# Optimization experiments

Measured on AMD Instinct MI355X. Metric: run time of the kernel, lower is better.

Reference implementation:

```python
import jax, jax.numpy as jnp
import numpy as np

N = 10000      # nodes
E = 320000     # edges (before self-loops)
IN_DIM = 128
HID = 64
OUT = 32
HEADS = 8
NEG_SLOPE = 0.2  # PyG GATConv default leaky_relu slope


def gat_conv(x, W, a_src, a_dst, b, src, dst, num_nodes, heads, d):
    """One PyG-style GATConv layer (eval mode, concat=True).
    x: [N, F_in], W: [F_in, heads*d], a_src/a_dst: [heads, d], b: [heads*d]
    src/dst: [E'] int edge endpoints (self-loops already included).
    """
    h = (x @ W).reshape(num_nodes, heads, d)              # [N, H, D]
    alpha_s = jnp.sum(h * a_src, axis=-1)                 # [N, H]
    alpha_d = jnp.sum(h * a_dst, axis=-1)                 # [N, H]
    logits = jax.nn.leaky_relu(alpha_s[src] + alpha_d[dst], NEG_SLOPE)  # [E', H]
    # segment softmax over incoming edges of each destination node
    m = jax.lax.stop_gradient(
        jax.ops.segment_max(logits, dst, num_segments=num_nodes))      # [N, H]
    e = jnp.exp(logits - m[dst])                          # [E', H]
    denom = jax.ops.segment_sum(e, dst, num_segments=num_nodes)        # [N, H]
    alpha = e / denom[dst]                                # [E', H]
    out = jax.ops.segment_sum(alpha[:, :, None] * h[src], dst,
                              num_segments=num_nodes)     # [N, H, D]
    return out.reshape(num_nodes, heads * d) + b


def setup_inputs() -> dict:
    key = jax.random.key(0)
    ks = jax.random.split(key, 10)
    x = jax.random.normal(ks[0], (N, IN_DIM), jnp.float32)
    edge_index = jax.random.randint(ks[1], (2, E), 0, N, dtype=jnp.int64)
    s1 = 1.0 / np.sqrt(IN_DIM)
    W1 = jax.random.normal(ks[2], (IN_DIM, HEADS * HID), jnp.float32) * s1
    a1_src = jax.random.normal(ks[3], (HEADS, HID), jnp.float32) * 0.1
    a1_dst = jax.random.normal(ks[4], (HEADS, HID), jnp.float32) * 0.1
    b1 = jnp.zeros((HEADS * HID,), jnp.float32)
    s2 = 1.0 / np.sqrt(HEADS * HID)
    W2 = jax.random.normal(ks[5], (HEADS * HID, OUT), jnp.float32) * s2
    a2_src = jax.random.normal(ks[6], (1, OUT), jnp.float32) * 0.1
    a2_dst = jax.random.normal(ks[7], (1, OUT), jnp.float32) * 0.1
    b2 = jnp.zeros((OUT,), jnp.float32)
    return {"x": x, "edge_index": edge_index,
            "W1": W1, "a1_src": a1_src, "a1_dst": a1_dst, "b1": b1,
            "W2": W2, "a2_src": a2_src, "a2_dst": a2_dst, "b2": b2}


def reference(x, edge_index, W1, a1_src, a1_dst, b1, W2, a2_src, a2_dst, b2):
    # add self-loops (PyG GATConv default add_self_loops=True)
    loops = jnp.arange(N, dtype=edge_index.dtype)
    src = jnp.concatenate([edge_index[0], loops])
    dst = jnp.concatenate([edge_index[1], loops])
    # dropout layers are identity in eval mode
    h = gat_conv(x, W1, a1_src, a1_dst, b1, src, dst, N, HEADS, HID)
    h = jax.nn.elu(h)
    out = gat_conv(h, W2, a2_src, a2_dst, b2, src, dst, N, 1, OUT)
    return out
```

## Files before the change

kernel.cpp:

```cpp
#include <hip/hip_runtime.h>
#include <math.h>

#define N_NODES 10000
#define E_EDGES 320000
#define EA      (E_EDGES + N_NODES)
#define IN_DIM  128
#define HID     512
#define HEADS   8
#define OUT_DIM 32
#define NEG     0.2f
#define CAP     160
#define KSPLIT  384
#define N_PAD   10048
#define NRB     628
#define RB_SH   6144

#define ZB   40
#define PXB  5024
#define PWB  256
#define SCB  645

typedef __attribute__((ext_vector_type(8))) short bf16x8;
typedef __attribute__((ext_vector_type(4))) float f32x4;

__device__ __forceinline__ float leaky(float x){ return x > 0.f ? x : NEG * x; }

__device__ __forceinline__ unsigned short bf16rn(float x){
    unsigned int b = __float_as_uint(x);
    b += 0x7fffu + ((b >> 16) & 1u);
    return (unsigned short)(b >> 16);
}

__device__ __forceinline__ size_t frag_off(int rb, int kk, int l15){
    int ks  = kk >> 5;
    int grp = (kk >> 3) & 3;
    int el  = kk & 7;
    return ((size_t)rb * RB_SH) + ((ks * 4 + grp) * 16 + l15) * 8 + el;
}

__global__ void k_pre(const float* __restrict__ x, const float* __restrict__ W1,
                      int* __restrict__ cnt,
                      unsigned short* __restrict__ Ax, unsigned short* __restrict__ Bt){
    int b = blockIdx.x, t = threadIdx.x;
    if (b < ZB){
        int i = b * 256 + t;
        if (i < N_NODES) cnt[i] = 0;
    } else if (b < ZB + PXB){
        int idx = (b - ZB) * 256 + t;
        int n = idx >> 7, k = idx & 127;
        float v = (n < N_NODES) ? x[(size_t)n * IN_DIM + k] : 0.f;
        unsigned short hi = bf16rn(v);
        float vhi = __uint_as_float((unsigned)hi << 16);
        unsigned short lo = bf16rn(v - vhi);
        int rb = n >> 4, l15 = n & 15;
        Ax[frag_off(rb, k, l15)]       = hi;
        Ax[frag_off(rb, 128 + k, l15)] = lo;
        Ax[frag_off(rb, 256 + k, l15)] = hi;
    } else {
        int idx = (b - ZB - PXB) * 256 + t;
        int nn = idx >> 7, k = idx & 127;
        float v = W1[(size_t)k * HID + nn];
        unsigned short hi = bf16rn(v);
        float vhi = __uint_as_float((unsigned)hi << 16);
        unsigned short lo = bf16rn(v - vhi);
        int nb = nn >> 4, l15 = nn & 15;
        Bt[frag_off(nb, k, l15)]       = hi;
        Bt[frag_off(nb, 128 + k, l15)] = hi;
        Bt[frag_off(nb, 256 + k, l15)] = lo;
    }
}

__launch_bounds__(512)
__global__ void k_sg(const int* __restrict__ eidx, int* __restrict__ cnt,
                     int* __restrict__ esrc,
                     const unsigned short* __restrict__ Ax,
                     const unsigned short* __restrict__ Bt,
                     const float* __restrict__ a1s, const float* __restrict__ a1d,
                     unsigned short* __restrict__ h1,
                     float* __restrict__ as1, float* __restrict__ ad1){
    if (blockIdx.x < SCB){
        int e = blockIdx.x * 512 + threadIdx.x;
        if (e < EA){
            int d, s;
            if (e < E_EDGES){ s = eidx[e]; d = eidx[E_EDGES + e]; }
            else { s = d = e - E_EDGES; }
            int pos = atomicAdd(&cnt[d], 1);
            if (pos < CAP) esrc[d * CAP + pos] = s;
        }
        return;
    }
    int rb = blockIdx.x - SCB;
    int by = threadIdx.x >> 6;
    int lane = threadIdx.x & 63;
    int l15 = lane & 15, grp = lane >> 4;
    int m0 = rb * 16;
    int n0 = by * 64;
    const unsigned short* ap = Ax + (size_t)rb * RB_SH + (size_t)lane * 8;
    bf16x8 a[12];
#pragma unroll
    for (int ks = 0; ks < 12; ks++)
        a[ks] = *reinterpret_cast<const bf16x8*>(ap + ks * 512);
    const unsigned short* bp = Bt + (size_t)(by * 4) * RB_SH + (size_t)lane * 8;
    f32x4 acc[4] = {};
#pragma unroll
    for (int ks = 0; ks < 12; ks++){
#pragma unroll
        for (int ns = 0; ns < 4; ns++){
            bf16x8 b = *reinterpret_cast<const bf16x8*>(bp + (size_t)ns * RB_SH + ks * 512);
            acc[ns] = __builtin_amdgcn_mfma_f32_16x16x32_bf16(a[ks], b, acc[ns], 0, 0, 0);
        }
    }
    float vs[4] = {0.f, 0.f, 0.f, 0.f}, vd[4] = {0.f, 0.f, 0.f, 0.f};
#pragma unroll
    for (int ns = 0; ns < 4; ns++){
        int c = n0 + ns * 16 + l15;
        float a_s = a1s[c], a_d = a1d[c];
#pragma unroll
        for (int r = 0; r < 4; r++){
            float v = acc[ns][r];
            int rr = m0 + grp * 4 + r;
            if (rr < N_NODES) h1[(size_t)rr * HID + c] = bf16rn(v);
            vs[r] += v * a_s; vd[r] += v * a_d;
        }
    }
#pragma unroll
    for (int r = 0; r < 4; r++){
#pragma unroll
        for (int off = 8; off >= 1; off >>= 1){
            vs[r] += __shfl_xor(vs[r], off);
            vd[r] += __shfl_xor(vd[r], off);
        }
    }
    if (l15 == 0){
#pragma unroll
        for (int r = 0; r < 4; r++){
            int rr = m0 + grp * 4 + r;
            if (rr < N_NODES){ as1[rr * HEADS + by] = vs[r]; ad1[rr * HEADS + by] = vd[r]; }
        }
    }
}

__launch_bounds__(128)
__global__ void k_agg1(const unsigned short* __restrict__ h1,
                       const float* __restrict__ as1, const float* __restrict__ ad1,
                       const int* __restrict__ cnt, const int* __restrict__ esrc,
                       const float* __restrict__ b1, float* __restrict__ h1b){
    int n = blockIdx.x;
    int c = cnt[n]; if (c > CAP) c = CAP;
    int beg = n * CAP;
    int t = threadIdx.x;
    __shared__ int   s_src[CAP];
    __shared__ float s_w[HEADS][CAP + 1];
    __shared__ float s_adn[HEADS];
    __shared__ float s_red[2][HEADS];
    __shared__ float s_m[HEADS];
    if (t < HEADS) s_adn[t] = ad1[n * HEADS + t];
    __syncthreads();
    float pm[HEADS];
#pragma unroll
    for (int h = 0; h < HEADS; h++) pm[h] = -INFINITY;
    for (int i = t; i < c; i += 128){
        int s = esrc[beg + i];
        float4 alo = *reinterpret_cast<const float4*>(as1 + (size_t)s * HEADS);
        float4 ahi = *reinterpret_cast<const float4*>(as1 + (size_t)s * HEADS + 4);
        float lg[HEADS];
        lg[0] = leaky(alo.x + s_adn[0]); lg[1] = leaky(alo.y + s_adn[1]);
        lg[2] = leaky(alo.z + s_adn[2]); lg[3] = leaky(alo.w + s_adn[3]);
        lg[4] = leaky(ahi.x + s_adn[4]); lg[5] = leaky(ahi.y + s_adn[5]);
        lg[6] = leaky(ahi.z + s_adn[6]); lg[7] = leaky(ahi.w + s_adn[7]);
        s_src[i] = s;
#pragma unroll
        for (int h = 0; h < HEADS; h++){ s_w[h][i] = lg[h]; pm[h] = fmaxf(pm[h], lg[h]); }
    }
#pragma unroll
    for (int h = 0; h < HEADS; h++)
#pragma unroll
        for (int off = 32; off >= 1; off >>= 1)
            pm[h] = fmaxf(pm[h], __shfl_down(pm[h], off));
    int wv = t >> 6;
    if ((t & 63) == 0)
#pragma unroll
        for (int h = 0; h < HEADS; h++) s_red[wv][h] = pm[h];
    __syncthreads();
    if (t < HEADS) s_m[t] = fmaxf(s_red[0][t], s_red[1][t]);
    __syncthreads();
    for (int i = t; i < c; i += 128){
#pragma unroll
        for (int h = 0; h < HEADS; h++) s_w[h][i] = __expf(s_w[h][i] - s_m[h]);
    }
    __syncthreads();
    int d0 = 4 * t;
    int h = t >> 4;
    float a0a = 0.f, a1a = 0.f, a2a = 0.f, a3a = 0.f, dena = 0.f;
    float a0b = 0.f, a1b = 0.f, a2b = 0.f, a3b = 0.f, denb = 0.f;
    int i = 0;
    for (; i + 1 < c; i += 2){
        float wa = s_w[h][i];     int sa = s_src[i];
        float wb = s_w[h][i + 1]; int sb = s_src[i + 1];
        uint2 hva = *reinterpret_cast<const uint2*>(h1 + (size_t)sa * HID + d0);
        uint2 hvb = *reinterpret_cast<const uint2*>(h1 + (size_t)sb * HID + d0);
        a0a += wa * __uint_as_float(hva.x << 16);
        a1a += wa * __uint_as_float(hva.x & 0xffff0000u);
        a2a += wa * __uint_as_float(hva.y << 16);
        a3a += wa * __uint_as_float(hva.y & 0xffff0000u);
        dena += wa;
        a0b += wb * __uint_as_float(hvb.x << 16);
        a1b += wb * __uint_as_float(hvb.x & 0xffff0000u);
        a2b += wb * __uint_as_float(hvb.y << 16);
        a3b += wb * __uint_as_float(hvb.y & 0xffff0000u);
        denb += wb;
    }
    if (i < c){
        float w = s_w[h][i]; int s = s_src[i];
        uint2 hv = *reinterpret_cast<const uint2*>(h1 + (size_t)s * HID + d0);
        a0a += w * __uint_as_float(hv.x << 16);
        a1a += w * __uint_as_float(hv.x & 0xffff0000u);
        a2a += w * __uint_as_float(hv.y << 16);
        a3a += w * __uint_as_float(hv.y & 0xffff0000u);
        dena += w;
    }
    float acc0 = a0a + a0b, acc1 = a1a + a1b, acc2 = a2a + a2b, acc3 = a3a + a3b;
    float den = dena + denb;
    float4 bv = *reinterpret_cast<const float4*>(b1 + d0);
    float rd = 1.f / den;
    float o0 = acc0 * rd + bv.x;
    float o1 = acc1 * rd + bv.y;
    float o2 = acc2 * rd + bv.z;
    float o3 = acc3 * rd + bv.w;
    float4 o;
    o.x = o0 > 0.f ? o0 : expm1f(o0);
    o.y = o1 > 0.f ? o1 : expm1f(o1);
    o.z = o2 > 0.f ? o2 : expm1f(o2);
    o.w = o3 > 0.f ? o3 : expm1f(o3);
    *reinterpret_cast<float4*>(h1b + (size_t)n * HID + d0) = o;
}

__launch_bounds__(128)
__global__ void k_gemm2(const float* __restrict__ h1b, const float* __restrict__ W2,
                        const float* __restrict__ a2s, const float* __restrict__ a2d,
                        float* __restrict__ h2, float* __restrict__ as2,
                        float* __restrict__ ad2){
    __shared__ float hs[16 * 516];
    int t = threadIdx.x;
    int n0 = blockIdx.x * 16;
    const float4* src = reinterpret_cast<const float4*>(h1b + (size_t)n0 * HID);
    for (int i = t; i < 2048; i += 128){
        int r = i >> 7, c4 = i & 127;
        *reinterpret_cast<float4*>(&hs[r * 516 + c4 * 4]) = src[i];
    }
    __syncthreads();
    int nl = t >> 3, cg = t & 7, c0 = cg * 4;
    float a0 = 0.f, a1 = 0.f, a2 = 0.f, a3 = 0.f;
#pragma unroll 2
    for (int k4 = 0; k4 < 128; k4++){
        float4 hv = *reinterpret_cast<const float4*>(&hs[nl * 516 + k4 * 4]);
        float4 w0 = *reinterpret_cast<const float4*>(W2 + (k4 * 4 + 0) * OUT_DIM + c0);
        float4 w1 = *reinterpret_cast<const float4*>(W2 + (k4 * 4 + 1) * OUT_DIM + c0);
        float4 w2 = *reinterpret_cast<const float4*>(W2 + (k4 * 4 + 2) * OUT_DIM + c0);
        float4 w3 = *reinterpret_cast<const float4*>(W2 + (k4 * 4 + 3) * OUT_DIM + c0);
        a0 += hv.x * w0.x + hv.y * w1.x + hv.z * w2.x + hv.w * w3.x;
        a1 += hv.x * w0.y + hv.y * w1.y + hv.z * w2.y + hv.w * w3.y;
        a2 += hv.x * w0.z + hv.y * w1.z + hv.z * w2.z + hv.w * w3.z;
        a3 += hv.x * w0.w + hv.y * w1.w + hv.z * w2.w + hv.w * w3.w;
    }
    float4 o; o.x = a0; o.y = a1; o.z = a2; o.w = a3;
    *reinterpret_cast<float4*>(h2 + (size_t)(n0 + nl) * OUT_DIM + c0) = o;
    float4 s4 = *reinterpret_cast<const float4*>(a2s + c0);
    float4 d4 = *reinterpret_cast<const float4*>(a2d + c0);
    float vs = a0 * s4.x + a1 * s4.y + a2 * s4.z + a3 * s4.w;
    float vd = a0 * d4.x + a1 * d4.y + a2 * d4.z + a3 * d4.w;
#pragma unroll
    for (int off = 4; off >= 1; off >>= 1){
        vs += __shfl_xor(vs, off);
        vd += __shfl_xor(vd, off);
    }
    if (cg == 0){ as2[n0 + nl] = vs; ad2[n0 + nl] = vd; }
}

__launch_bounds__(256)
__global__ void k_agg2(const float* __restrict__ h2, const float* __restrict__ as2,
                       const float* __restrict__ ad2, const int* __restrict__ cnt,
                       const int* __restrict__ esrc,
                       const float* __restrict__ b2, float* __restrict__ out){
    int wv = threadIdx.x >> 6;
    int lane = threadIdx.x & 63;
    int n = blockIdx.x * 4 + wv;
    __shared__ float s_w[4][CAP];
    __shared__ int   s_src[4][CAP];
    int c = cnt[n]; if (c > CAP) c = CAP;
    int beg = n * CAP;
    float adn = ad2[n];
    float pm = -INFINITY;
    for (int i = lane; i < c; i += 64){
        int s = esrc[beg + i];
        float lg = leaky(as2[s] + adn);
        s_src[wv][i] = s; s_w[wv][i] = lg;
        pm = fmaxf(pm, lg);
    }
#pragma unroll
    for (int off = 32; off >= 1; off >>= 1)
        pm = fmaxf(pm, __shfl_xor(pm, off));
    __syncthreads();
    for (int i = lane; i < c; i += 64) s_w[wv][i] = __expf(s_w[wv][i] - pm);
    __syncthreads();
    int d = lane & 31, half = lane >> 5;
    float acc = 0.f, den = 0.f;
    for (int i = half; i < c; i += 2){
        float w = s_w[wv][i]; int s = s_src[wv][i];
        acc += w * h2[(size_t)s * OUT_DIM + d];
        den += w;
    }
    acc += __shfl_xor(acc, 32);
    den += __shfl_xor(den, 32);
    if (lane < OUT_DIM) out[(size_t)n * OUT_DIM + d] = acc / den + b2[d];
}

extern "C" void kernel_launch(void* const* d_in, const int* in_sizes, int n_in,
                              void* d_out, int out_size, void* d_ws, size_t ws_size,
                              hipStream_t stream){
    const float* x   = (const float*)d_in[0];
    const int*  eidx = (const int*)  d_in[1];
    const float* W1  = (const float*)d_in[2];
    const float* a1s = (const float*)d_in[3];
    const float* a1d = (const float*)d_in[4];
    const float* b1  = (const float*)d_in[5];
    const float* W2  = (const float*)d_in[6];
    const float* a2s = (const float*)d_in[7];
    const float* a2d = (const float*)d_in[8];
    const float* b2  = (const float*)d_in[9];
    float* out = (float*)d_out;

    char* ws = (char*)d_ws;
    size_t off = 0;
    auto alloc = [&](size_t bytes) -> void* {
        void* p = ws + off;
        off += (bytes + 255) & ~(size_t)255;
        return p;
    };
    unsigned short* h1 = (unsigned short*)alloc((size_t)N_NODES * HID * 2);
    float* h1b  = (float*)alloc((size_t)N_NODES * HID * 4);
    float* as1  = (float*)alloc((size_t)N_NODES * HEADS * 4);
    float* ad1  = (float*)alloc((size_t)N_NODES * HEADS * 4);
    float* h2   = (float*)alloc((size_t)N_NODES * OUT_DIM * 4);
    float* vs2  = (float*)alloc((size_t)N_NODES * 4);
    float* vd2  = (float*)alloc((size_t)N_NODES * 4);
    int* cnt    = (int*)alloc((size_t)N_NODES * 4);
    int* esrc   = (int*)alloc((size_t)N_NODES * CAP * 4);
    unsigned short* Bt = (unsigned short*)alloc((size_t)32 * RB_SH * 2);
    unsigned short* Ax = (unsigned short*)h1b;

    k_pre <<<ZB + PXB + PWB, 256, 0, stream>>>(x, W1, cnt, Ax, Bt);
    k_sg  <<<SCB + NRB, 512, 0, stream>>>(eidx, cnt, esrc, Ax, Bt, a1s, a1d,
                                          h1, as1, ad1);
    k_agg1<<<N_NODES, 128, 0, stream>>>(h1, as1, ad1, cnt, esrc, b1, h1b);
    k_gemm2<<<N_NODES / 16, 128, 0, stream>>>(h1b, W2, a2s, a2d, h2, vs2, vd2);
    k_agg2<<<N_NODES / 4, 256, 0, stream>>>(h2, vs2, vd2, cnt, esrc, b2, out);
}
```

Baseline: 132.8 us.

## Fuse layer-2 GEMM into aggregation and store split-bf16 hi/lo operands compactly

Folds the second-layer projection (h1 row times W2) into the first aggregation kernel, using a pre-transposed W2 copy, so the fp32 h1b intermediate is never written and read back and one launch is dropped. The preprocessing kernel now stages x and W1 tiles through shared memory and writes packed 16-byte hi/lo fragments. It stores hi and lo once each instead of three duplicated slices. The GEMM issues three MFMAs per step, reusing registers for the split terms. The fused per-node matvec adds work to each aggregation block, and this may cost occupancy.

New measurement: 155.9 us. 17.3% more time.

```diff
diff --git a/kernel.cpp b/kernel.cpp
--- a/kernel.cpp
+++ b/kernel.cpp
@@ -10,14 +10,13 @@
 #define OUT_DIM 32
 #define NEG     0.2f
 #define CAP     160
-#define KSPLIT  384
 #define N_PAD   10048
 #define NRB     628
-#define RB_SH   6144
-
-#define ZB   40
-#define PXB  5024
-#define PWB  256
+#define RB_SH   4096
+
+#define PWB  32
+#define PTB  64
+#define ZBK  40
 #define SCB  645
 
 typedef __attribute__((ext_vector_type(8))) short bf16x8;
@@ -31,42 +30,74 @@
     return (unsigned short)(b >> 16);
 }
 
-__device__ __forceinline__ size_t frag_off(int rb, int kk, int l15){
-    int ks  = kk >> 5;
-    int grp = (kk >> 3) & 3;
-    int el  = kk & 7;
-    return ((size_t)rb * RB_SH) + ((ks * 4 + grp) * 16 + l15) * 8 + el;
-}
-
 __global__ void k_pre(const float* __restrict__ x, const float* __restrict__ W1,
-                      int* __restrict__ cnt,
-                      unsigned short* __restrict__ Ax, unsigned short* __restrict__ Bt){
+                      const float* __restrict__ W2, int* __restrict__ cnt,
+                      unsigned short* __restrict__ Ax, unsigned short* __restrict__ Bt,
+                      float* __restrict__ W2T){
     int b = blockIdx.x, t = threadIdx.x;
-    if (b < ZB){
-        int i = b * 256 + t;
+    if (b < NRB){
+        __shared__ float xs[16 * 132];
+        int rb = b;
+#pragma unroll
+        for (int j = 0; j < 2; j++){
+            int idx = t + j * 256;
+            int r = idx >> 5, c4 = idx & 31;
+            int row = rb * 16 + r;
+            float4 v = make_float4(0.f, 0.f, 0.f, 0.f);
+            if (row < N_NODES)
+                v = *reinterpret_cast<const float4*>(x + (size_t)row * IN_DIM + c4 * 4);
+            *reinterpret_cast<float4*>(&xs[r * 132 + c4 * 4]) = v;
+        }
+        __syncthreads();
+        int l15 = t & 15, kk8 = t >> 4;
+        unsigned short hi[8], lo[8];
+#pragma unroll
+        for (int el = 0; el < 8; el++){
+            float f = xs[l15 * 132 + kk8 * 8 + el];
+            hi[el] = bf16rn(f);
+            lo[el] = bf16rn(f - __uint_as_float((unsigned)hi[el] << 16));
+        }
+        uint4 H, L;
+        H.x = hi[0] | ((unsigned)hi[1] << 16); H.y = hi[2] | ((unsigned)hi[3] << 16);
+        H.z = hi[4] | ((unsigned)hi[5] << 16); H.w = hi[6] | ((unsigned)hi[7] << 16);
+        L.x = lo[0] | ((unsigned)lo[1] << 16); L.y = lo[2] | ((unsigned)lo[3] << 16);
+        L.z = lo[4] | ((unsigned)lo[5] << 16); L.w = lo[6] | ((unsigned)lo[7] << 16);
+        unsigned short* base = Ax + (size_t)rb * RB_SH;
+        *reinterpret_cast<uint4*>(base + (kk8 * 16 + l15) * 8) = H;
+        *reinterpret_cast<uint4*>(base + 2048 + (kk8 * 16 + l15) * 8) = L;
+    } else if (b < NRB + PWB){
+        __shared__ float ws[128 * 17];
+        int nb = b - NRB;
+        int j = t & 15, kr = t >> 4;
+#pragma unroll
+        for (int it = 0; it < 8; it++){
+            int k = it * 16 + kr;
+            ws[k * 17 + j] = W1[(size_t)k * HID + nb * 16 + j];
+        }
+        __syncthreads();
+        int l15 = t & 15, kk8 = t >> 4;
+        unsigned short hi[8], lo[8];
+#pragma unroll
+        for (int el = 0; el < 8; el++){
+            float f = ws[(kk8 * 8 + el) * 17 + l15];
+            hi[el] = bf16rn(f);
+            lo[el] = bf16rn(f - __uint_as_float((unsigned)hi[el] << 16));
+        }
+        uint4 H, L;
+        H.x = hi[0] | ((unsigned)hi[1] << 16); H.y = hi[2] | ((unsigned)hi[3] << 16);
+        H.z = hi[4] | ((unsigned)hi[5] << 16); H.w = hi[6] | ((unsigned)hi[7] << 16);
+        L.x = lo[0] | ((unsigned)lo[1] << 16); L.y = lo[2] | ((unsigned)lo[3] << 16);
+        L.z = lo[4] | ((unsigned)lo[5] << 16); L.w = lo[6] | ((unsigned)lo[7] << 16);
+        unsigned short* base = Bt + (size_t)nb * RB_SH;
+        *reinterpret_cast<uint4*>(base + (kk8 * 16 + l15) * 8) = H;
+        *reinterpret_cast<uint4*>(base + 2048 + (kk8 * 16 + l15) * 8) = L;
+    } else if (b < NRB + PWB + PTB){
+        int idx = (b - NRB - PWB) * 256 + t;
+        int k = idx & 511, c = idx >> 9;
+        W2T[(size_t)c * HID + k] = W2[(size_t)k * OUT_DIM + c];
+    } else {
+        int i = (b - NRB - PWB - PTB) * 256 + t;
         if (i < N_NODES) cnt[i] = 0;
-    } else if (b < ZB + PXB){
-        int idx = (b - ZB) * 256 + t;
-        int n = idx >> 7, k = idx & 127;
-        float v = (n < N_NODES) ? x[(size_t)n * IN_DIM + k] : 0.f;
-        unsigned short hi = bf16rn(v);
-        float vhi = __uint_as_float((unsigned)hi << 16);
-        unsigned short lo = bf16rn(v - vhi);
-        int rb = n >> 4, l15 = n & 15;
-        Ax[frag_off(rb, k, l15)]       = hi;
-        Ax[frag_off(rb, 128 + k, l15)] = lo;
-        Ax[frag_off(rb, 256 + k, l15)] = hi;
-    } else {
-        int idx = (b - ZB - PXB) * 256 + t;
-        int nn = idx >> 7, k = idx & 127;
-        float v = W1[(size_t)k * HID + nn];
-        unsigned short hi = bf16rn(v);
-        float vhi = __uint_as_float((unsigned)hi << 16);
-        unsigned short lo = bf16rn(v - vhi);
-        int nb = nn >> 4, l15 = nn & 15;
-        Bt[frag_off(nb, k, l15)]       = hi;
-        Bt[frag_off(nb, 128 + k, l15)] = hi;
-        Bt[frag_off(nb, 256 + k, l15)] = lo;
     }
 }
 
@@ -96,18 +127,24 @@
     int m0 = rb * 16;
     int n0 = by * 64;
     const unsigned short* ap = Ax + (size_t)rb * RB_SH + (size_t)lane * 8;
-    bf16x8 a[12];
-#pragma unroll
-    for (int ks = 0; ks < 12; ks++)
-        a[ks] = *reinterpret_cast<const bf16x8*>(ap + ks * 512);
+    bf16x8 a_hi[4], a_lo[4];
+#pragma unroll
+    for (int ks = 0; ks < 4; ks++){
+        a_hi[ks] = *reinterpret_cast<const bf16x8*>(ap + ks * 512);
+        a_lo[ks] = *reinterpret_cast<const bf16x8*>(ap + 2048 + ks * 512);
+    }
     const unsigned short* bp = Bt + (size_t)(by * 4) * RB_SH + (size_t)lane * 8;
     f32x4 acc[4] = {};
 #pragma unroll
-    for (int ks = 0; ks < 12; ks++){
+    for (int ks = 0; ks < 4; ks++){
 #pragma unroll
         for (int ns = 0; ns < 4; ns++){
-            bf16x8 b = *reinterpret_cast<const bf16x8*>(bp + (size_t)ns * RB_SH + ks * 512);
-            acc[ns] = __builtin_amdgcn_mfma_f32_16x16x32_bf16(a[ks], b, acc[ns], 0, 0, 0);
+            const unsigned short* bb = bp + (size_t)ns * RB_SH + ks * 512;
+            bf16x8 b_hi = *reinterpret_cast<const bf16x8*>(bb);
+            bf16x8 b_lo = *reinterpret_cast<const bf16x8*>(bb + 2048);
+            acc[ns] = __builtin_amdgcn_mfma_f32_16x16x32_bf16(a_hi[ks], b_hi, acc[ns], 0, 0, 0);
+            acc[ns] = __builtin_amdgcn_mfma_f32_16x16x32_bf16(a_lo[ks], b_hi, acc[ns], 0, 0, 0);
+            acc[ns] = __builtin_amdgcn_mfma_f32_16x16x32_bf16(a_hi[ks], b_lo, acc[ns], 0, 0, 0);
         }
     }
     float vs[4] = {0.f, 0.f, 0.f, 0.f}, vd[4] = {0.f, 0.f, 0.f, 0.f};
@@ -144,7 +181,10 @@
 __global__ void k_agg1(const unsigned short* __restrict__ h1,
                        const float* __restrict__ as1, const float* __restrict__ ad1,
                        const int* __restrict__ cnt, const int* __restrict__ esrc,
-                       const float* __restrict__ b1, float* __restrict__ h1b){
+                       const float* __restrict__ b1, const float* __restrict__ W2T,
+                       const float* __restrict__ a2s, const float* __restrict__ a2d,
+                       float* __restrict__ h2, float* __restrict__ vs2,
+                       float* __restrict__ vd2){
     int n = blockIdx.x;
     int c = cnt[n]; if (c > CAP) c = CAP;
     int beg = n * CAP;
@@ -154,6 +194,8 @@
     __shared__ float s_adn[HEADS];
     __shared__ float s_red[2][HEADS];
     __shared__ float s_m[HEADS];
+    __shared__ float s_row[HID];
+    __shared__ float s_p[4][OUT_DIM];
     if (t < HEADS) s_adn[t] = ad1[n * HEADS + t];
     __syncthreads();
     float pm[HEADS];
@@ -191,90 +233,67 @@
     __syncthreads();
     int d0 = 4 * t;
     int h = t >> 4;
-    float a0a = 0.f, a1a = 0.f, a2a = 0.f, a3a = 0.f, dena = 0.f;
-    float a0b = 0.f, a1b = 0.f, a2b = 0.f, a3b = 0.f, denb = 0.f;
+    float ac[4][4] = {}, dn[4] = {};
     int i = 0;
-    for (; i + 1 < c; i += 2){
-        float wa = s_w[h][i];     int sa = s_src[i];
-        float wb = s_w[h][i + 1]; int sb = s_src[i + 1];
-        uint2 hva = *reinterpret_cast<const uint2*>(h1 + (size_t)sa * HID + d0);
-        uint2 hvb = *reinterpret_cast<const uint2*>(h1 + (size_t)sb * HID + d0);
-        a0a += wa * __uint_as_float(hva.x << 16);
-        a1a += wa * __uint_as_float(hva.x & 0xffff0000u);
-        a2a += wa * __uint_as_float(hva.y << 16);
-        a3a += wa * __uint_as_float(hva.y & 0xffff0000u);
-        dena += wa;
-        a0b += wb * __uint_as_float(hvb.x << 16);
-        a1b += wb * __uint_as_float(hvb.x & 0xffff0000u);
-        a2b += wb * __uint_as_float(hvb.y << 16);
-        a3b += wb * __uint_as_float(hvb.y & 0xffff0000u);
-        denb += wb;
-    }
-    if (i < c){
+    for (; i + 3 < c; i += 4){
+#pragma unroll
+        for (int u = 0; u < 4; u++){
+            float w = s_w[h][i + u]; int s = s_src[i + u];
+            uint2 hv = *reinterpret_cast<const uint2*>(h1 + (size_t)s * HID + d0);
+            ac[u][0] += w * __uint_as_float(hv.x << 16);
+            ac[u][1] += w * __uint_as_float(hv.x & 0xffff0000u);
+            ac[u][2] += w * __uint_as_float(hv.y << 16);
+            ac[u][3] += w * __uint_as_float(hv.y & 0xffff0000u);
+            dn[u] += w;
+        }
+    }
+    for (; i < c; i++){
         float w = s_w[h][i]; int s = s_src[i];
         uint2 hv = *reinterpret_cast<const uint2*>(h1 + (size_t)s * HID + d0);
-        a0a += w * __uint_as_float(hv.x << 16);
-        a1a += w * __uint_as_float(hv.x & 0xffff0000u);
-        a2a += w * __uint_as_float(hv.y << 16);
-        a3a += w * __uint_as_float(hv.y & 0xffff0000u);
-        dena += w;
-    }
-    float acc0 = a0a + a0b, acc1 = a1a + a1b, acc2 = a2a + a2b, acc3 = a3a + a3b;
-    float den = dena + denb;
+        ac[0][0] += w * __uint_as_float(hv.x << 16);
+        ac[0][1] += w * __uint_as_float(hv.x & 0xffff0000u);
+        ac[0][2] += w * __uint_as_float(hv.y << 16);
+        ac[0][3] += w * __uint_as_float(hv.y & 0xffff0000u);
+        dn[0] += w;
+    }
+    float den = (dn[0] + dn[1]) + (dn[2] + dn[3]);
+    float rd = 1.f / den;
     float4 bv = *reinterpret_cast<const float4*>(b1 + d0);
-    float rd = 1.f / den;
-    float o0 = acc0 * rd + bv.x;
-    float o1 = acc1 * rd + bv.y;
-    float o2 = acc2 * rd + bv.z;
-    float o3 = acc3 * rd + bv.w;
+    float o0 = ((ac[0][0] + ac[1][0]) + (ac[2][0] + ac[3][0])) * rd + bv.x;
+    float o1 = ((ac[0][1] + ac[1][1]) + (ac[2][1] + ac[3][1])) * rd + bv.y;
+    float o2 = ((ac[0][2] + ac[1][2]) + (ac[2][2] + ac[3][2])) * rd + bv.z;
+    float o3 = ((ac[0][3] + ac[1][3]) + (ac[2][3] + ac[3][3])) * rd + bv.w;
     float4 o;
     o.x = o0 > 0.f ? o0 : expm1f(o0);
     o.y = o1 > 0.f ? o1 : expm1f(o1);
     o.z = o2 > 0.f ? o2 : expm1f(o2);
     o.w = o3 > 0.f ? o3 : expm1f(o3);
-    *reinterpret_cast<float4*>(h1b + (size_t)n * HID + d0) = o;
-}
-
-__launch_bounds__(128)
-__global__ void k_gemm2(const float* __restrict__ h1b, const float* __restrict__ W2,
-                        const float* __restrict__ a2s, const float* __restrict__ a2d,
-                        float* __restrict__ h2, float* __restrict__ as2,
-                        float* __restrict__ ad2){
-    __shared__ float hs[16 * 516];
-    int t = threadIdx.x;
-    int n0 = blockIdx.x * 16;
-    const float4* src = reinterpret_cast<const float4*>(h1b + (size_t)n0 * HID);
-    for (int i = t; i < 2048; i += 128){
-        int r = i >> 7, c4 = i & 127;
-        *reinterpret_cast<float4*>(&hs[r * 516 + c4 * 4]) = src[i];
-    }
-    __syncthreads();
-    int nl = t >> 3, cg = t & 7, c0 = cg * 4;
-    float a0 = 0.f, a1 = 0.f, a2 = 0.f, a3 = 0.f;
-#pragma unroll 2
-    for (int k4 = 0; k4 < 128; k4++){
-        float4 hv = *reinterpret_cast<const float4*>(&hs[nl * 516 + k4 * 4]);
-        float4 w0 = *reinterpret_cast<const float4*>(W2 + (k4 * 4 + 0) * OUT_DIM + c0);
-        float4 w1 = *reinterpret_cast<const float4*>(W2 + (k4 * 4 + 1) * OUT_DIM + c0);
-        float4 w2 = *reinterpret_cast<const float4*>(W2 + (k4 * 4 + 2) * OUT_DIM + c0);
-        float4 w3 = *reinterpret_cast<const float4*>(W2 + (k4 * 4 + 3) * OUT_DIM + c0);
-        a0 += hv.x * w0.x + hv.y * w1.x + hv.z * w2.x + hv.w * w3.x;
-        a1 += hv.x * w0.y + hv.y * w1.y + hv.z * w2.y + hv.w * w3.y;
-        a2 += hv.x * w0.z + hv.y * w1.z + hv.z * w2.z + hv.w * w3.z;
-        a3 += hv.x * w0.w + hv.y * w1.w + hv.z * w2.w + hv.w * w3.w;
-    }
-    float4 o; o.x = a0; o.y = a1; o.z = a2; o.w = a3;
-    *reinterpret_cast<float4*>(h2 + (size_t)(n0 + nl) * OUT_DIM + c0) = o;
-    float4 s4 = *reinterpret_cast<const float4*>(a2s + c0);
-    float4 d4 = *reinterpret_cast<const float4*>(a2d + c0);
-    float vs = a0 * s4.x + a1 * s4.y + a2 * s4.z + a3 * s4.w;
-    float vd = a0 * d4.x + a1 * d4.y + a2 * d4.z + a3 * d4.w;
-#pragma unroll
-    for (int off = 4; off >= 1; off >>= 1){
-        vs += __shfl_xor(vs, off);
-        vd += __shfl_xor(vd, off);
-    }
-    if (cg == 0){ as2[n0 + nl] = vs; ad2[n0 + nl] = vd; }
+    *reinterpret_cast<float4*>(&s_row[d0]) = o;
+    __syncthreads();
+    int cc = t & 31, q = t >> 5;
+    const float4* wr = reinterpret_cast<const float4*>(W2T + (size_t)cc * HID + q * 128);
+    const float4* rr = reinterpret_cast<const float4*>(&s_row[q * 128]);
+    float p = 0.f;
+#pragma unroll 8
+    for (int kk = 0; kk < 32; kk++){
+        float4 rv = rr[kk];
+        float4 wv = wr[kk];
+        p += rv.x * wv.x + rv.y * wv.y + rv.z * wv.z + rv.w * wv.w;
+    }
+    s_p[q][cc] = p;
+    __syncthreads();
+    if (t < OUT_DIM){
+        float h2c = (s_p[0][t] + s_p[1][t]) + (s_p[2][t] + s_p[3][t]);
+        h2[(size_t)n * OUT_DIM + t] = h2c;
+        float vs = h2c * a2s[t];
+        float vd = h2c * a2d[t];
+#pragma unroll
+        for (int off = 16; off >= 1; off >>= 1){
+            vs += __shfl_xor(vs, off);
+            vd += __shfl_xor(vd, off);
+        }
+        if (t == 0){ vs2[n] = vs; vd2[n] = vd; }
+    }
 }
 
 __launch_bounds__(256)
@@ -338,7 +357,9 @@
         return p;
     };
     unsigned short* h1 = (unsigned short*)alloc((size_t)N_NODES * HID * 2);
-    float* h1b  = (float*)alloc((size_t)N_NODES * HID * 4);
+    unsigned short* Ax = (unsigned short*)alloc((size_t)NRB * RB_SH * 2);
+    unsigned short* Bt = (unsigned short*)alloc((size_t)32 * RB_SH * 2);
+    float* W2T  = (float*)alloc((size_t)OUT_DIM * HID * 4);
     float* as1  = (float*)alloc((size_t)N_NODES * HEADS * 4);
     float* ad1  = (float*)alloc((size_t)N_NODES * HEADS * 4);
     float* h2   = (float*)alloc((size_t)N_NODES * OUT_DIM * 4);
@@ -346,13 +367,11 @@
     float* vd2  = (float*)alloc((size_t)N_NODES * 4);
     int* cnt    = (int*)alloc((size_t)N_NODES * 4);
     int* esrc   = (int*)alloc((size_t)N_NODES * CAP * 4);
-    unsigned short* Bt = (unsigned short*)alloc((size_t)32 * RB_SH * 2);
-    unsigned short* Ax = (unsigned short*)h1b;
-
-    k_pre <<<ZB + PXB + PWB, 256, 0, stream>>>(x, W1, cnt, Ax, Bt);
+
+    k_pre <<<NRB + PWB + PTB + ZBK, 256, 0, stream>>>(x, W1, W2, cnt, Ax, Bt, W2T);
     k_sg  <<<SCB + NRB, 512, 0, stream>>>(eidx, cnt, esrc, Ax, Bt, a1s, a1d,
                                           h1, as1, ad1);
-    k_agg1<<<N_NODES, 128, 0, stream>>>(h1, as1, ad1, cnt, esrc, b1, h1b);
-    k_gemm2<<<N_NODES / 16, 128, 0, stream>>>(h1b, W2, a2s, a2d, h2, vs2, vd2);
+    k_agg1<<<N_NODES, 128, 0, stream>>>(h1, as1, ad1, cnt, esrc, b1, W2T,
+                                        a2s, a2d, h2, vs2, vd2);
     k_agg2<<<N_NODES / 4, 256, 0, stream>>>(h2, vs2, vd2, cnt, esrc, b2, out);
 }
```

## Store hi/lo bf16 split once and vectorize fragment packing via shared memory

Applied to the files above, without the earlier changes.

The preprocessing kernel now stages x and W1 tiles in shared memory and writes packed 16-byte MFMA fragments, replacing per-element scattered 2-byte stores. The triplicated K=384 layout (hi,lo,hi / hi,hi,lo) is replaced by a K=256 hi/lo layout. The GEMM issues the three split-bf16 MFMAs explicitly per k-step. This shrinks the fragment buffers and cuts uncoalesced writes in the prep kernel, at the cost of extra shared-memory staging and a barrier.

Result: faster. 126.8 us (-4.5%).

```diff
diff --git a/kernel.cpp b/kernel.cpp
--- a/kernel.cpp
+++ b/kernel.cpp
@@ -10,14 +10,12 @@
 #define OUT_DIM 32
 #define NEG     0.2f
 #define CAP     160
-#define KSPLIT  384
 #define N_PAD   10048
 #define NRB     628
-#define RB_SH   6144
-
-#define ZB   40
-#define PXB  5024
-#define PWB  256
+#define RB_SH   4096
+
+#define PWB  32
+#define ZBK  40
 #define SCB  645
 
 typedef __attribute__((ext_vector_type(8))) short bf16x8;
@@ -31,42 +29,69 @@
     return (unsigned short)(b >> 16);
 }
 
-__device__ __forceinline__ size_t frag_off(int rb, int kk, int l15){
-    int ks  = kk >> 5;
-    int grp = (kk >> 3) & 3;
-    int el  = kk & 7;
-    return ((size_t)rb * RB_SH) + ((ks * 4 + grp) * 16 + l15) * 8 + el;
-}
-
 __global__ void k_pre(const float* __restrict__ x, const float* __restrict__ W1,
                       int* __restrict__ cnt,
                       unsigned short* __restrict__ Ax, unsigned short* __restrict__ Bt){
     int b = blockIdx.x, t = threadIdx.x;
-    if (b < ZB){
-        int i = b * 256 + t;
+    if (b < NRB){
+        __shared__ float xs[16 * 132];
+        int rb = b;
+#pragma unroll
+        for (int j = 0; j < 2; j++){
+            int idx = t + j * 256;
+            int r = idx >> 5, c4 = idx & 31;
+            int row = rb * 16 + r;
+            float4 v = make_float4(0.f, 0.f, 0.f, 0.f);
+            if (row < N_NODES)
+                v = *reinterpret_cast<const float4*>(x + (size_t)row * IN_DIM + c4 * 4);
+            *reinterpret_cast<float4*>(&xs[r * 132 + c4 * 4]) = v;
+        }
+        __syncthreads();
+        int l15 = t & 15, kk8 = t >> 4;
+        unsigned short hi[8], lo[8];
+#pragma unroll
+        for (int el = 0; el < 8; el++){
+            float f = xs[l15 * 132 + kk8 * 8 + el];
+            hi[el] = bf16rn(f);
+            lo[el] = bf16rn(f - __uint_as_float((unsigned)hi[el] << 16));
+        }
+        uint4 H, L;
+        H.x = hi[0] | ((unsigned)hi[1] << 16); H.y = hi[2] | ((unsigned)hi[3] << 16);
+        H.z = hi[4] | ((unsigned)hi[5] << 16); H.w = hi[6] | ((unsigned)hi[7] << 16);
+        L.x = lo[0] | ((unsigned)lo[1] << 16); L.y = lo[2] | ((unsigned)lo[3] << 16);
+        L.z = lo[4] | ((unsigned)lo[5] << 16); L.w = lo[6] | ((unsigned)lo[7] << 16);
+        unsigned short* base = Ax + (size_t)rb * RB_SH;
+        *reinterpret_cast<uint4*>(base + (kk8 * 16 + l15) * 8) = H;
+        *reinterpret_cast<uint4*>(base + 2048 + (kk8 * 16 + l15) * 8) = L;
+    } else if (b < NRB + PWB){
+        __shared__ float wsh[128 * 17];
+        int nb = b - NRB;
+        int j = t & 15, kr = t >> 4;
+#pragma unroll
+        for (int it = 0; it < 8; it++){
+            int k = it * 16 + kr;
+            wsh[k * 17 + j] = W1[(size_t)k * HID + nb * 16 + j];
+        }
+        __syncthreads();
+        int l15 = t & 15, kk8 = t >> 4;
+        unsigned short hi[8], lo[8];
+#pragma unroll
+        for (int el = 0; el < 8; el++){
+            float f = wsh[(kk8 * 8 + el) * 17 + l15];
+            hi[el] = bf16rn(f);
+            lo[el] = bf16rn(f - __uint_as_float((unsigned)hi[el] << 16));
+        }
+        uint4 H, L;
+        H.x = hi[0] | ((unsigned)hi[1] << 16); H.y = hi[2] | ((unsigned)hi[3] << 16);
+        H.z = hi[4] | ((unsigned)hi[5] << 16); H.w = hi[6] | ((unsigned)hi[7] << 16);
+        L.x = lo[0] | ((unsigned)lo[1] << 16); L.y = lo[2] | ((unsigned)lo[3] << 16);
+        L.z = lo[4] | ((unsigned)lo[5] << 16); L.w = lo[6] | ((unsigned)lo[7] << 16);
+        unsigned short* base = Bt + (size_t)nb * RB_SH;
+        *reinterpret_cast<uint4*>(base + (kk8 * 16 + l15) * 8) = H;
+        *reinterpret_cast<uint4*>(base + 2048 + (kk8 * 16 + l15) * 8) = L;
+    } else {
+        int i = (b - NRB - PWB) * 256 + t;
         if (i < N_NODES) cnt[i] = 0;
-    } else if (b < ZB + PXB){
-        int idx = (b - ZB) * 256 + t;
-        int n = idx >> 7, k = idx & 127;
-        float v = (n < N_NODES) ? x[(size_t)n * IN_DIM + k] : 0.f;
-        unsigned short hi = bf16rn(v);
-        float vhi = __uint_as_float((unsigned)hi << 16);
-        unsigned short lo = bf16rn(v - vhi);
-        int rb = n >> 4, l15 = n & 15;
-        Ax[frag_off(rb, k, l15)]       = hi;
-        Ax[frag_off(rb, 128 + k, l15)] = lo;
-        Ax[frag_off(rb, 256 + k, l15)] = hi;
-    } else {
-        int idx = (b - ZB - PXB) * 256 + t;
-        int nn = idx >> 7, k = idx & 127;
-        float v = W1[(size_t)k * HID + nn];
-        unsigned short hi = bf16rn(v);
-        float vhi = __uint_as_float((unsigned)hi << 16);
-        unsigned short lo = bf16rn(v - vhi);
-        int nb = nn >> 4, l15 = nn & 15;
-        Bt[frag_off(nb, k, l15)]       = hi;
-        Bt[frag_off(nb, 128 + k, l15)] = hi;
-        Bt[frag_off(nb, 256 + k, l15)] = lo;
     }
 }
 
@@ -96,18 +121,24 @@
     int m0 = rb * 16;
     int n0 = by * 64;
     const unsigned short* ap = Ax + (size_t)rb * RB_SH + (size_t)lane * 8;
-    bf16x8 a[12];
-#pragma unroll
-    for (int ks = 0; ks < 12; ks++)
-        a[ks] = *reinterpret_cast<const bf16x8*>(ap + ks * 512);
+    bf16x8 a_hi[4], a_lo[4];
+#pragma unroll
+    for (int ks = 0; ks < 4; ks++){
+        a_hi[ks] = *reinterpret_cast<const bf16x8*>(ap + ks * 512);
+        a_lo[ks] = *reinterpret_cast<const bf16x8*>(ap + 2048 + ks * 512);
+    }
     const unsigned short* bp = Bt + (size_t)(by * 4) * RB_SH + (size_t)lane * 8;
     f32x4 acc[4] = {};
 #pragma unroll
-    for (int ks = 0; ks < 12; ks++){
+    for (int ks = 0; ks < 4; ks++){
 #pragma unroll
         for (int ns = 0; ns < 4; ns++){
-            bf16x8 b = *reinterpret_cast<const bf16x8*>(bp + (size_t)ns * RB_SH + ks * 512);
-            acc[ns] = __builtin_amdgcn_mfma_f32_16x16x32_bf16(a[ks], b, acc[ns], 0, 0, 0);
+            const unsigned short* bb = bp + (size_t)ns * RB_SH + ks * 512;
+            bf16x8 b_hi = *reinterpret_cast<const bf16x8*>(bb);
+            bf16x8 b_lo = *reinterpret_cast<const bf16x8*>(bb + 2048);
+            acc[ns] = __builtin_amdgcn_mfma_f32_16x16x32_bf16(a_hi[ks], b_hi, acc[ns], 0, 0, 0);
+            acc[ns] = __builtin_amdgcn_mfma_f32_16x16x32_bf16(a_lo[ks], b_hi, acc[ns], 0, 0, 0);
+            acc[ns] = __builtin_amdgcn_mfma_f32_16x16x32_bf16(a_hi[ks], b_lo, acc[ns], 0, 0, 0);
         }
     }
     float vs[4] = {0.f, 0.f, 0.f, 0.f}, vd[4] = {0.f, 0.f, 0.f, 0.f};
@@ -339,6 +370,7 @@
     };
     unsigned short* h1 = (unsigned short*)alloc((size_t)N_NODES * HID * 2);
     float* h1b  = (float*)alloc((size_t)N_NODES * HID * 4);
+    unsigned short* Bt = (unsigned short*)alloc((size_t)32 * RB_SH * 2);
     float* as1  = (float*)alloc((size_t)N_NODES * HEADS * 4);
     float* ad1  = (float*)alloc((size_t)N_NODES * HEADS * 4);
     float* h2   = (float*)alloc((size_t)N_NODES * OUT_DIM * 4);
@@ -346,10 +378,9 @@
     float* vd2  = (float*)alloc((size_t)N_NODES * 4);
     int* cnt    = (int*)alloc((size_t)N_NODES * 4);
     int* esrc   = (int*)alloc((size_t)N_NODES * CAP * 4);
-    unsigned short* Bt = (unsigned short*)alloc((size_t)32 * RB_SH * 2);
     unsigned short* Ax = (unsigned short*)h1b;
 
-    k_pre <<<ZB + PXB + PWB, 256, 0, stream>>>(x, W1, cnt, Ax, Bt);
+    k_pre <<<NRB + PWB + ZBK, 256, 0, stream>>>(x, W1, cnt, Ax, Bt);
     k_sg  <<<SCB + NRB, 512, 0, stream>>>(eidx, cnt, esrc, Ax, Bt, a1s, a1d,
                                           h1, as1, ad1);
     k_agg1<<<N_NODES, 128, 0, stream>>>(h1, as1, ad1, cnt, esrc, b1, h1b);
```
